# Performance work log

Measured on AMD Instinct MI355X. Metric: run time of the kernel, lower is better.

The kernel has to match this reference:

```python
import jax, jax.numpy as jnp
import numpy as np

TOPK = 2
ALPHA = 32.0
EPS = 1e-20


def setup_inputs() -> dict:
    key = jax.random.key(0)
    ks = jax.random.split(key, 6)
    E, D, R, Q, V = 16, 2048, 16, 2048, 512
    B, S = 2, 2048
    return {
        "hidden_states": jax.random.normal(ks[0], (B, S, D), jnp.float32),
        "router_weight": jax.random.normal(ks[1], (E, D), jnp.float32) * 0.02,
        "q_lora_a": jax.random.normal(ks[2], (E, D, R), jnp.float32) * 0.02,
        "q_lora_b": jax.random.normal(ks[3], (E, R, Q), jnp.float32) * 0.02,
        "v_lora_a": jax.random.normal(ks[4], (E, D, R), jnp.float32) * 0.02,
        "v_lora_b": jax.random.normal(ks[5], (E, R, V), jnp.float32) * 0.02,
    }


def reference(hidden_states, router_weight, q_lora_a, q_lora_b, v_lora_a, v_lora_b):
    E, D, R = q_lora_a.shape
    Qo = q_lora_b.shape[-1]
    Vo = v_lora_b.shape[-1]
    scale = ALPHA / float(R)
    orig_shape = hidden_states.shape[:-1]
    h = hidden_states.reshape(-1, D)  # [n, D]
    n = h.shape[0]

    # router: top-k softmax probs, renormalized over the k selected experts
    logits = jnp.einsum('nd,ed->ne', h, router_weight)
    probs = jax.nn.softmax(logits, axis=-1)
    scores, idx = jax.lax.top_k(probs, TOPK)          # [n, k]
    scores = scores / (scores.sum(-1, keepdims=True) + EPS)

    # per-token expert combine weights c[n, e] = scale * sum_k score_k * 1[idx_k == e]
    c = jnp.zeros((n, E), h.dtype).at[jnp.arange(n)[:, None], idx].add(scores * scale)

    # dense per-expert low-rank projections; weighting by c makes non-selected
    # experts contribute zero -> identical math to gather + einsum + weighted sum.
    q_low = jnp.einsum('nd,edr->ner', h, q_lora_a) * c[..., None]  # [n, E, R]
    v_low = jnp.einsum('nd,edr->ner', h, v_lora_a) * c[..., None]
    q_delta = jnp.einsum('ner,erq->nq', q_low, q_lora_b)
    v_delta = jnp.einsum('ner,erv->nv', v_low, v_lora_b)

    return (q_delta.reshape(*orig_shape, Qo), v_delta.reshape(*orig_shape, Vo))
```

## Files before the change

### kernel.cpp

```cpp
#include <hip/hip_runtime.h>
#include <math.h>

#define DD 2048
#define EE 16
#define RR 16
#define QO 2048
#define VO 512
#define DSPLIT 4
#define DRANGE (DD / DSPLIT)
#define DC 64
#define HSTR (DC + 4)
#define ASTR 20
#define RDC 256
#define DSPL 8
#define TB 32
#define ACHUNKS 16
#define T2 32
#define CGQ (QO / 256)
#define CGV (VO / 256)

struct Route { int i0, i1; float w0, w1; };

__global__ void zero_cnt(int* __restrict__ cnt) {
    if (threadIdx.x < EE) cnt[threadIdx.x] = 0;
}

__global__ __launch_bounds__(256) void logits_kernel(
    const float* __restrict__ h, const float* __restrict__ rw,
    double* __restrict__ lgp, int n)
{
    __shared__ float hs[8 * RDC];

    int t0 = blockIdx.x * 8;
    int ds = blockIdx.y;
    int d0 = ds * RDC;
    int e  = threadIdx.x >> 4;
    int l  = threadIdx.x & 15;

    for (int i = threadIdx.x; i < 8 * (RDC / 4); i += 256) {
        int t = i >> 6, dq = (i & 63) * 4;
        float4 v = make_float4(0.f, 0.f, 0.f, 0.f);
        if (t0 + t < n)
            v = *(const float4*)&h[(size_t)(t0 + t) * DD + d0 + dq];
        *(float4*)&hs[t * RDC + dq] = v;
    }
    __syncthreads();

    double acc[8];
#pragma unroll
    for (int t = 0; t < 8; ++t) acc[t] = 0.0;

    const float* rwe = rw + e * DD + d0;
#pragma unroll
    for (int g = 0; g < RDC / 64; ++g) {
        int d = g * 64 + l * 4;
        float4 r4 = *(const float4*)&rwe[d];
        double rx = r4.x, ry = r4.y, rz = r4.z, rw4 = r4.w;
#pragma unroll
        for (int t = 0; t < 8; ++t) {
            float4 hv = *(const float4*)&hs[t * RDC + d];
            acc[t] += (double)hv.x * rx + (double)hv.y * ry
                    + (double)hv.z * rz + (double)hv.w * rw4;
        }
    }
#pragma unroll
    for (int t = 0; t < 8; ++t) {
#pragma unroll
        for (int off = 8; off; off >>= 1)
            acc[t] += __shfl_down(acc[t], off, 16);
    }
    if (l == 0) {
#pragma unroll
        for (int t = 0; t < 8; ++t) {
            int tok = t0 + t;
            if (tok < n)
                lgp[((size_t)tok * DSPL + ds) * EE + e] = acc[t];
        }
    }
}

__global__ __launch_bounds__(256) void finalize_kernel(
    const double* __restrict__ lgp, Route* __restrict__ route,
    unsigned short* __restrict__ bucket, int* __restrict__ cnt, int n)
{
    int tok = blockIdx.x * 256 + threadIdx.x;
    if (tok >= n) return;

    double lg[EE];
#pragma unroll
    for (int e = 0; e < EE; ++e) lg[e] = 0.0;
    const double* p = lgp + (size_t)tok * (DSPL * EE);
#pragma unroll
    for (int ds = 0; ds < DSPL; ++ds)
#pragma unroll
        for (int e = 0; e < EE; ++e) lg[e] += p[ds * EE + e];

    int i0 = 0;
    for (int i = 1; i < EE; ++i) if (lg[i] > lg[i0]) i0 = i;
    int i1 = -1;
    for (int i = 0; i < EE; ++i)
        if (i != i0 && (i1 < 0 || lg[i] > lg[i1])) i1 = i;
    double ed = exp(lg[i1] - lg[i0]);
    double w0 = 2.0 / (1.0 + ed);
    Route rt;
    rt.i0 = i0; rt.i1 = i1;
    rt.w0 = (float)w0;
    rt.w1 = (float)(2.0 - w0);
    route[tok] = rt;
    int p0 = atomicAdd(&cnt[i0], 1);
    bucket[(size_t)i0 * n + p0] = (unsigned short)(tok * 2);
    int p1 = atomicAdd(&cnt[i1], 1);
    bucket[(size_t)i1 * n + p1] = (unsigned short)(tok * 2 + 1);
}

__global__ __launch_bounds__(256) void a_kernel(
    const float* __restrict__ h, const Route* __restrict__ route,
    const unsigned short* __restrict__ bucket, const int* __restrict__ cnt,
    const float* __restrict__ qa, const float* __restrict__ va,
    float* __restrict__ low, int n)
{
    int e  = blockIdx.x;
    int ds = blockIdx.z;
    int cnt_e = cnt[e];

    __shared__ int   sel_tok[TB];
    __shared__ int   sel_k[TB];
    __shared__ float sel_w[TB];
    __align__(16) __shared__ float aq_s[DC * ASTR];
    __align__(16) __shared__ float av_s[DC * ASTR];
    __align__(16) __shared__ float hs[TB * HSTR];

    const float* qa_e = qa + (size_t)e * DD * RR;
    const float* va_e = va + (size_t)e * DD * RR;

    int s    = threadIdx.x & 15;
    int tile = threadIdx.x >> 4;
    int tp   = tile >> 2;
    int rp   = tile & 3;

    for (int c0 = blockIdx.y * TB; c0 < cnt_e; c0 += gridDim.y * TB) {
        int mb = min(TB, cnt_e - c0);
        if (threadIdx.x < TB && threadIdx.x < mb) {
            int slot = bucket[(size_t)e * n + c0 + threadIdx.x];
            int tok = slot >> 1, k = slot & 1;
            Route rt = route[tok];
            sel_tok[threadIdx.x] = tok;
            sel_k[threadIdx.x]   = k;
            sel_w[threadIdx.x]   = k ? rt.w1 : rt.w0;
        }
        float accq[8][4], accv[8][4];
#pragma unroll
        for (int ti = 0; ti < 8; ++ti)
#pragma unroll
            for (int ri = 0; ri < 4; ++ri) { accq[ti][ri] = 0.f; accv[ti][ri] = 0.f; }

        for (int d0 = ds * DRANGE; d0 < (ds + 1) * DRANGE; d0 += DC) {
            __syncthreads();
            {
                int i = threadIdx.x;
                int d = i >> 2, rf = (i & 3) * 4;
                *(float4*)&aq_s[d * ASTR + rf] = *(const float4*)&qa_e[(size_t)(d0 + d) * RR + rf];
                *(float4*)&av_s[d * ASTR + rf] = *(const float4*)&va_e[(size_t)(d0 + d) * RR + rf];
            }
            for (int i = threadIdx.x; i < TB * (DC / 4); i += 256) {
                int j = i >> 4, dq = (i & 15) * 4;
                float4 v = make_float4(0.f, 0.f, 0.f, 0.f);
                if (j < mb)
                    v = *(const float4*)&h[(size_t)sel_tok[j] * DD + d0 + dq];
                *(float4*)&hs[j * HSTR + dq] = v;
            }
            __syncthreads();
#pragma unroll
            for (int dd = 0; dd < DC / 16; ++dd) {
                int d = (dd << 4) + s;
                float hv[8];
#pragma unroll
                for (int ti = 0; ti < 8; ++ti)
                    hv[ti] = hs[(tp * 8 + ti) * HSTR + d];
                float4 aqv = *(const float4*)&aq_s[d * ASTR + rp * 4];
                float4 avv = *(const float4*)&av_s[d * ASTR + rp * 4];
                const float* aqp = &aqv.x;
                const float* avp = &avv.x;
#pragma unroll
                for (int ti = 0; ti < 8; ++ti)
#pragma unroll
                    for (int ri = 0; ri < 4; ++ri) {
                        accq[ti][ri] = fmaf(hv[ti], aqp[ri], accq[ti][ri]);
                        accv[ti][ri] = fmaf(hv[ti], avp[ri], accv[ti][ri]);
                    }
            }
        }
#pragma unroll
        for (int ti = 0; ti < 8; ++ti)
#pragma unroll
            for (int ri = 0; ri < 4; ++ri) {
#pragma unroll
                for (int off = 8; off; off >>= 1) {
                    accq[ti][ri] += __shfl_down(accq[ti][ri], off, 16);
                    accv[ti][ri] += __shfl_down(accv[ti][ri], off, 16);
                }
            }
        if (s == 0) {
#pragma unroll
            for (int ti = 0; ti < 8; ++ti) {
                int t = tp * 8 + ti;
                if (t < mb) {
                    int   tok = sel_tok[t];
                    int   k   = sel_k[t];
                    float w   = sel_w[t];
                    size_t base = ((size_t)(tok * 2 + k) * DSPLIT + ds) * 32;
                    float4 q4 = make_float4(accq[ti][0] * w, accq[ti][1] * w,
                                            accq[ti][2] * w, accq[ti][3] * w);
                    float4 v4 = make_float4(accv[ti][0] * w, accv[ti][1] * w,
                                            accv[ti][2] * w, accv[ti][3] * w);
                    *(float4*)&low[base + rp * 4]      = q4;
                    *(float4*)&low[base + 16 + rp * 4] = v4;
                }
            }
        }
        __syncthreads();
    }
}

__global__ __launch_bounds__(256) void b_kernel(
    const Route* __restrict__ route, const float* __restrict__ low,
    const float* __restrict__ qb, const float* __restrict__ vb,
    float* __restrict__ outq, float* __restrict__ outv, int n)
{
    int t0 = blockIdx.x * T2;
    int cg = blockIdx.y;
    int tid = threadIdx.x;

    __shared__ float acc_s[T2 * 256];
    __shared__ float ls[T2 * 2 * RR];
    __shared__ int   elist[EE * T2];
    __shared__ int   ecnt[EE];
    __shared__ Route rts[T2];

    if (tid < EE) ecnt[tid] = 0;
    if (tid < T2) {
        int tok = t0 + tid;
        if (tok < n) rts[tid] = route[tok];
        else { rts[tid].i0 = -1; rts[tid].i1 = -1; rts[tid].w0 = 0.f; rts[tid].w1 = 0.f; }
    }
    __syncthreads();
    if (tid < T2 * 2) {
        int j = tid >> 1, k = tid & 1;
        int e = k ? rts[j].i1 : rts[j].i0;
        if (e >= 0) {
            int p = atomicAdd(&ecnt[e], 1);
            elist[e * T2 + p] = j * 2 + k;
        }
    }
    int side = (cg >= CGQ) ? 1 : 0;
    {
        int slot = tid >> 2, r4 = (tid & 3) * 4;
        int j = slot >> 1, k = slot & 1;
        int tok = t0 + j;
        float4 v = make_float4(0.f, 0.f, 0.f, 0.f);
        if (tok < n) {
            const float* lp = low + (size_t)(tok * 2 + k) * (DSPLIT * 32) + side * 16 + r4;
            float4 p0 = *(const float4*)(lp);
            float4 p1 = *(const float4*)(lp + 32);
            float4 p2 = *(const float4*)(lp + 64);
            float4 p3 = *(const float4*)(lp + 96);
            v.x = p0.x + p1.x + p2.x + p3.x;
            v.y = p0.y + p1.y + p2.y + p3.y;
            v.z = p0.z + p1.z + p2.z + p3.z;
            v.w = p0.w + p1.w + p2.w + p3.w;
        }
        *(float4*)&ls[slot * RR + r4] = v;
    }
#pragma unroll
    for (int j = 0; j < T2; ++j) acc_s[j * 256 + tid] = 0.f;
    __syncthreads();

    const float* bp; float* outp; int W, colbase;
    if (cg < CGQ) { bp = qb; outp = outq; W = QO; colbase = cg * 256; }
    else          { bp = vb; outp = outv; W = VO; colbase = (cg - CGQ) * 256; }
    int col = colbase + tid;

    float bcA[RR], bcB[RR];
    {
        const float* be = bp + col;
#pragma unroll
        for (int r = 0; r < RR; ++r) bcA[r] = be[(size_t)r * W];
    }

#define PROC_E(EI, BC)                                                      \
    {                                                                       \
        int c = ecnt[EI];                                                   \
        for (int ii = 0; ii < c; ++ii) {                                    \
            int sk = elist[(EI) * T2 + ii];                                 \
            const float* lp = &ls[sk * RR];                                 \
            float4 l0 = *(const float4*)(lp);                               \
            float4 l1 = *(const float4*)(lp + 4);                           \
            float4 l2 = *(const float4*)(lp + 8);                           \
            float4 l3 = *(const float4*)(lp + 12);                          \
            float v = 0.f;                                                  \
            v = fmaf(l0.x, BC[0],  v); v = fmaf(l0.y, BC[1],  v);           \
            v = fmaf(l0.z, BC[2],  v); v = fmaf(l0.w, BC[3],  v);           \
            v = fmaf(l1.x, BC[4],  v); v = fmaf(l1.y, BC[5],  v);           \
            v = fmaf(l1.z, BC[6],  v); v = fmaf(l1.w, BC[7],  v);           \
            v = fmaf(l2.x, BC[8],  v); v = fmaf(l2.y, BC[9],  v);           \
            v = fmaf(l2.z, BC[10], v); v = fmaf(l2.w, BC[11], v);           \
            v = fmaf(l3.x, BC[12], v); v = fmaf(l3.y, BC[13], v);           \
            v = fmaf(l3.z, BC[14], v); v = fmaf(l3.w, BC[15], v);           \
            acc_s[(sk >> 1) * 256 + tid] += v;   \
        }                                                                   \
    }

    for (int e = 0; e < EE; e += 2) {
        {
            const float* bn = bp + (size_t)(e + 1) * RR * W + col;
#pragma unroll
            for (int r = 0; r < RR; ++r) bcB[r] = bn[(size_t)r * W];
        }
        PROC_E(e, bcA);
        if (e + 2 < EE) {
            const float* bn = bp + (size_t)(e + 2) * RR * W + col;
#pragma unroll
            for (int r = 0; r < RR; ++r) bcA[r] = bn[(size_t)r * W];
        }
        PROC_E(e + 1, bcB);
    }
#undef PROC_E

#pragma unroll
    for (int j = 0; j < T2; ++j) {
        int tok = t0 + j;
        if (tok < n) outp[(size_t)tok * W + col] = acc_s[j * 256 + tid];
    }
}

extern "C" void kernel_launch(void* const* d_in, const int* in_sizes, int n_in,
                              void* d_out, int out_size, void* d_ws, size_t ws_size,
                              hipStream_t stream) {
    const float* h  = (const float*)d_in[0];
    const float* rw = (const float*)d_in[1];
    const float* qa = (const float*)d_in[2];
    const float* qb = (const float*)d_in[3];
    const float* va = (const float*)d_in[4];
    const float* vb = (const float*)d_in[5];

    int n = in_sizes[0] / DD;
    float* out  = (float*)d_out;
    float* outq = out;
    float* outv = out + (size_t)n * QO;

    char* ws = (char*)d_ws;
    Route* route = (Route*)ws;
    size_t off = ((size_t)n * sizeof(Route) + 255) & ~(size_t)255;
    int* cnt = (int*)(ws + off);
    off = (off + EE * sizeof(int) + 255) & ~(size_t)255;
    unsigned short* bucket = (unsigned short*)(ws + off);
    off = (off + (size_t)EE * n * sizeof(unsigned short) + 255) & ~(size_t)255;
    float* low = (float*)(ws + off);
    double* lgp = (double*)low;

    zero_cnt<<<1, 64, 0, stream>>>(cnt);

    dim3 g1((n + 7) / 8, DSPL);
    logits_kernel<<<g1, 256, 0, stream>>>(h, rw, lgp, n);

    finalize_kernel<<<(n + 255) / 256, 256, 0, stream>>>(lgp, route, bucket, cnt, n);

    dim3 g2(EE, ACHUNKS, DSPLIT);
    a_kernel<<<g2, 256, 0, stream>>>(h, route, bucket, cnt, qa, va, low, n);

    dim3 g3((n + T2 - 1) / T2, CGQ + CGV);
    b_kernel<<<g3, 256, 0, stream>>>(route, low, qb, vb, outq, outv, n);
}
```

Before: 240.6 us.

## Restructure routing finalize and A-projection kernel; fold counter reset into logits kernel

Removes the separate counter-zeroing launch by resetting the counts inside the logits kernel. The finalize kernel now uses 16 lanes per token with shuffle reductions for the top-2 search. The A kernel preloads the whole per-expert D-slice of both LoRA A matrices into shared memory once. Each wave then streams its own 8 tokens' hidden rows straight from global memory into registers with double buffering, which removes the per-chunk block syncs and the hidden-state staging. Risks: the in-kernel counter reset only works if finalize is strictly ordered after logits, register pressure rises, and the hidden-state reads are strided with less coalescing.

Result: no change. 236.7 us (-1.6%).

```diff
diff --git a/kernel.cpp b/kernel.cpp
--- a/kernel.cpp
+++ b/kernel.cpp
@@ -9,27 +9,24 @@
 #define DSPLIT 4
 #define DRANGE (DD / DSPLIT)
 #define DC 64
-#define HSTR (DC + 4)
-#define ASTR 20
 #define RDC 256
 #define DSPL 8
 #define TB 32
-#define ACHUNKS 16
+#define ABLK 8
 #define T2 32
 #define CGQ (QO / 256)
 #define CGV (VO / 256)
 
 struct Route { int i0, i1; float w0, w1; };
 
-__global__ void zero_cnt(int* __restrict__ cnt) {
-    if (threadIdx.x < EE) cnt[threadIdx.x] = 0;
-}
-
 __global__ __launch_bounds__(256) void logits_kernel(
     const float* __restrict__ h, const float* __restrict__ rw,
-    double* __restrict__ lgp, int n)
+    double* __restrict__ lgp, int* __restrict__ cnt, int n)
 {
     __shared__ float hs[8 * RDC];
+
+    if (blockIdx.x == 0 && blockIdx.y == 0 && threadIdx.x < EE)
+        cnt[threadIdx.x] = 0;
 
     int t0 = blockIdx.x * 8;
     int ds = blockIdx.y;
@@ -83,37 +80,78 @@
     const double* __restrict__ lgp, Route* __restrict__ route,
     unsigned short* __restrict__ bucket, int* __restrict__ cnt, int n)
 {
-    int tok = blockIdx.x * 256 + threadIdx.x;
+    int j   = threadIdx.x >> 4;
+    int l   = threadIdx.x & 15;
+    int tok = blockIdx.x * 16 + j;
     if (tok >= n) return;
 
-    double lg[EE];
-#pragma unroll
-    for (int e = 0; e < EE; ++e) lg[e] = 0.0;
-    const double* p = lgp + (size_t)tok * (DSPL * EE);
-#pragma unroll
-    for (int ds = 0; ds < DSPL; ++ds)
-#pragma unroll
-        for (int e = 0; e < EE; ++e) lg[e] += p[ds * EE + e];
-
-    int i0 = 0;
-    for (int i = 1; i < EE; ++i) if (lg[i] > lg[i0]) i0 = i;
-    int i1 = -1;
-    for (int i = 0; i < EE; ++i)
-        if (i != i0 && (i1 < 0 || lg[i] > lg[i1])) i1 = i;
-    double ed = exp(lg[i1] - lg[i0]);
-    double w0 = 2.0 / (1.0 + ed);
-    Route rt;
-    rt.i0 = i0; rt.i1 = i1;
-    rt.w0 = (float)w0;
-    rt.w1 = (float)(2.0 - w0);
-    route[tok] = rt;
-    int p0 = atomicAdd(&cnt[i0], 1);
-    bucket[(size_t)i0 * n + p0] = (unsigned short)(tok * 2);
-    int p1 = atomicAdd(&cnt[i1], 1);
-    bucket[(size_t)i1 * n + p1] = (unsigned short)(tok * 2 + 1);
-}
-
-__global__ __launch_bounds__(256) void a_kernel(
+    const double* p = lgp + (size_t)tok * (DSPL * EE) + l;
+    double s = 0.0;
+#pragma unroll
+    for (int ds = 0; ds < DSPL; ++ds) s += p[ds * EE];
+
+    double m1 = s; int i1 = l;
+#pragma unroll
+    for (int off = 8; off; off >>= 1) {
+        double om = __shfl_xor(m1, off, 16);
+        int    oi = __shfl_xor(i1, off, 16);
+        if (om > m1 || (om == m1 && oi < i1)) { m1 = om; i1 = oi; }
+    }
+    double s2 = (l == i1) ? -1.0e300 : s;
+    double m2 = s2; int i2 = l;
+#pragma unroll
+    for (int off = 8; off; off >>= 1) {
+        double om = __shfl_xor(m2, off, 16);
+        int    oi = __shfl_xor(i2, off, 16);
+        if (om > m2 || (om == m2 && oi < i2)) { m2 = om; i2 = oi; }
+    }
+    if (l == 0) {
+        double ed = exp(m2 - m1);
+        double w0 = 2.0 / (1.0 + ed);
+        Route rt;
+        rt.i0 = i1; rt.i1 = i2;
+        rt.w0 = (float)w0;
+        rt.w1 = (float)(2.0 - w0);
+        route[tok] = rt;
+        int p0 = atomicAdd(&cnt[i1], 1);
+        bucket[(size_t)i1 * n + p0] = (unsigned short)(tok * 2);
+        int p1 = atomicAdd(&cnt[i2], 1);
+        bucket[(size_t)i2 * n + p1] = (unsigned short)(tok * 2 + 1);
+    }
+}
+
+__device__ __forceinline__ void loadh(float (&hv)[4][8],
+        const float* const (&hp)[8], int d0) {
+#pragma unroll
+    for (int dd = 0; dd < 4; ++dd)
+#pragma unroll
+        for (int ti = 0; ti < 8; ++ti)
+            hv[dd][ti] = hp[ti][d0 + dd * 16];
+}
+
+__device__ __forceinline__ void computeh(float (&accq)[8][4], float (&accv)[8][4],
+        const float (&hv)[4][8], const float* aq, const float* av,
+        int d0, int s, int rp) {
+#pragma unroll
+    for (int dd = 0; dd < 4; ++dd) {
+        int d = d0 + dd * 16 + s;
+        float4 aqv = *(const float4*)&aq[d * RR + rp * 4];
+        float4 avv = *(const float4*)&av[d * RR + rp * 4];
+        const float* ap = &aqv.x;
+        const float* vp = &avv.x;
+#pragma unroll
+        for (int ti = 0; ti < 8; ++ti) {
+            float hvv = hv[dd][ti];
+#pragma unroll
+            for (int ri = 0; ri < 4; ++ri) {
+                accq[ti][ri] = fmaf(hvv, ap[ri], accq[ti][ri]);
+                accv[ti][ri] = fmaf(hvv, vp[ri], accv[ti][ri]);
+            }
+        }
+    }
+}
+
+__global__ __launch_bounds__(256, 2) void a_kernel(
     const float* __restrict__ h, const Route* __restrict__ route,
     const unsigned short* __restrict__ bucket, const int* __restrict__ cnt,
     const float* __restrict__ qa, const float* __restrict__ va,
@@ -122,74 +160,65 @@
     int e  = blockIdx.x;
     int ds = blockIdx.z;
     int cnt_e = cnt[e];
-
-    __shared__ int   sel_tok[TB];
-    __shared__ int   sel_k[TB];
-    __shared__ float sel_w[TB];
-    __align__(16) __shared__ float aq_s[DC * ASTR];
-    __align__(16) __shared__ float av_s[DC * ASTR];
-    __align__(16) __shared__ float hs[TB * HSTR];
-
-    const float* qa_e = qa + (size_t)e * DD * RR;
-    const float* va_e = va + (size_t)e * DD * RR;
-
-    int s    = threadIdx.x & 15;
-    int tile = threadIdx.x >> 4;
-    int tp   = tile >> 2;
-    int rp   = tile & 3;
-
-    for (int c0 = blockIdx.y * TB; c0 < cnt_e; c0 += gridDim.y * TB) {
-        int mb = min(TB, cnt_e - c0);
-        if (threadIdx.x < TB && threadIdx.x < mb) {
-            int slot = bucket[(size_t)e * n + c0 + threadIdx.x];
-            int tok = slot >> 1, k = slot & 1;
-            Route rt = route[tok];
-            sel_tok[threadIdx.x] = tok;
-            sel_k[threadIdx.x]   = k;
-            sel_w[threadIdx.x]   = k ? rt.w1 : rt.w0;
-        }
+    if ((int)(blockIdx.y * TB) >= cnt_e) return;
+
+    __align__(16) __shared__ float aq_s[DRANGE * RR];
+    __align__(16) __shared__ float av_s[DRANGE * RR];
+
+    const int dbase = ds * DRANGE;
+    const float* qa_e = qa + ((size_t)e * DD + dbase) * RR;
+    const float* va_e = va + ((size_t)e * DD + dbase) * RR;
+
+#pragma unroll
+    for (int k = 0; k < 8; ++k) {
+        int t = (k << 8) + threadIdx.x;
+        *(float4*)&aq_s[t * 4] = *(const float4*)&qa_e[(size_t)t * 4];
+        *(float4*)&av_s[t * 4] = *(const float4*)&va_e[(size_t)t * 4];
+    }
+    __syncthreads();
+
+    int lane = threadIdx.x & 63;
+    int w    = threadIdx.x >> 6;
+    int s    = lane & 15;
+    int rp   = lane >> 4;
+
+    for (int cb = blockIdx.y * TB; cb < cnt_e; cb += gridDim.y * TB) {
+        int cw = cb + w * 8;
+        if (cw >= cnt_e) continue;
+
+        int sl = 0; float wt = 0.f;
+        int idx = cw + lane;
+        if (lane < 8 && idx < cnt_e) {
+            sl = bucket[(size_t)e * n + idx];
+            Route rt = route[sl >> 1];
+            wt = (sl & 1) ? rt.w1 : rt.w0;
+        }
+        const float* hp[8];
+        int   slots[8];
+        float wts[8];
+#pragma unroll
+        for (int ti = 0; ti < 8; ++ti) {
+            slots[ti] = __shfl(sl, ti);
+            wts[ti]   = __shfl(wt, ti);
+            hp[ti]    = h + (size_t)(slots[ti] >> 1) * DD + dbase + s;
+        }
+
         float accq[8][4], accv[8][4];
 #pragma unroll
         for (int ti = 0; ti < 8; ++ti)
 #pragma unroll
             for (int ri = 0; ri < 4; ++ri) { accq[ti][ri] = 0.f; accv[ti][ri] = 0.f; }
 
-        for (int d0 = ds * DRANGE; d0 < (ds + 1) * DRANGE; d0 += DC) {
-            __syncthreads();
-            {
-                int i = threadIdx.x;
-                int d = i >> 2, rf = (i & 3) * 4;
-                *(float4*)&aq_s[d * ASTR + rf] = *(const float4*)&qa_e[(size_t)(d0 + d) * RR + rf];
-                *(float4*)&av_s[d * ASTR + rf] = *(const float4*)&va_e[(size_t)(d0 + d) * RR + rf];
-            }
-            for (int i = threadIdx.x; i < TB * (DC / 4); i += 256) {
-                int j = i >> 4, dq = (i & 15) * 4;
-                float4 v = make_float4(0.f, 0.f, 0.f, 0.f);
-                if (j < mb)
-                    v = *(const float4*)&h[(size_t)sel_tok[j] * DD + d0 + dq];
-                *(float4*)&hs[j * HSTR + dq] = v;
-            }
-            __syncthreads();
-#pragma unroll
-            for (int dd = 0; dd < DC / 16; ++dd) {
-                int d = (dd << 4) + s;
-                float hv[8];
-#pragma unroll
-                for (int ti = 0; ti < 8; ++ti)
-                    hv[ti] = hs[(tp * 8 + ti) * HSTR + d];
-                float4 aqv = *(const float4*)&aq_s[d * ASTR + rp * 4];
-                float4 avv = *(const float4*)&av_s[d * ASTR + rp * 4];
-                const float* aqp = &aqv.x;
-                const float* avp = &avv.x;
-#pragma unroll
-                for (int ti = 0; ti < 8; ++ti)
-#pragma unroll
-                    for (int ri = 0; ri < 4; ++ri) {
-                        accq[ti][ri] = fmaf(hv[ti], aqp[ri], accq[ti][ri]);
-                        accv[ti][ri] = fmaf(hv[ti], avp[ri], accv[ti][ri]);
-                    }
-            }
-        }
+        float hvA[4][8], hvB[4][8];
+        loadh(hvA, hp, 0);
+#pragma unroll
+        for (int d0 = 0; d0 < DRANGE; d0 += 2 * DC) {
+            loadh(hvB, hp, d0 + DC);
+            computeh(accq, accv, hvA, aq_s, av_s, d0, s, rp);
+            if (d0 + 2 * DC < DRANGE) loadh(hvA, hp, d0 + 2 * DC);
+            computeh(accq, accv, hvB, aq_s, av_s, d0 + DC, s, rp);
+        }
+
 #pragma unroll
         for (int ti = 0; ti < 8; ++ti)
 #pragma unroll
@@ -203,22 +232,19 @@
         if (s == 0) {
 #pragma unroll
             for (int ti = 0; ti < 8; ++ti) {
-                int t = tp * 8 + ti;
-                if (t < mb) {
-                    int   tok = sel_tok[t];
-                    int   k   = sel_k[t];
-                    float w   = sel_w[t];
-                    size_t base = ((size_t)(tok * 2 + k) * DSPLIT + ds) * 32;
-                    float4 q4 = make_float4(accq[ti][0] * w, accq[ti][1] * w,
-                                            accq[ti][2] * w, accq[ti][3] * w);
-                    float4 v4 = make_float4(accv[ti][0] * w, accv[ti][1] * w,
-                                            accv[ti][2] * w, accv[ti][3] * w);
+                if (cw + ti < cnt_e) {
+                    int   sl2 = slots[ti];
+                    float wt2 = wts[ti];
+                    size_t base = ((size_t)sl2 * DSPLIT + ds) * 32;
+                    float4 q4 = make_float4(accq[ti][0] * wt2, accq[ti][1] * wt2,
+                                            accq[ti][2] * wt2, accq[ti][3] * wt2);
+                    float4 v4 = make_float4(accv[ti][0] * wt2, accv[ti][1] * wt2,
+                                            accv[ti][2] * wt2, accv[ti][3] * wt2);
                     *(float4*)&low[base + rp * 4]      = q4;
                     *(float4*)&low[base + 16 + rp * 4] = v4;
                 }
             }
         }
-        __syncthreads();
     }
 }
 
@@ -358,14 +384,12 @@
     float* low = (float*)(ws + off);
     double* lgp = (double*)low;
 
-    zero_cnt<<<1, 64, 0, stream>>>(cnt);
-
     dim3 g1((n + 7) / 8, DSPL);
-    logits_kernel<<<g1, 256, 0, stream>>>(h, rw, lgp, n);
-
-    finalize_kernel<<<(n + 255) / 256, 256, 0, stream>>>(lgp, route, bucket, cnt, n);
-
-    dim3 g2(EE, ACHUNKS, DSPLIT);
+    logits_kernel<<<g1, 256, 0, stream>>>(h, rw, lgp, cnt, n);
+
+    finalize_kernel<<<(n + 15) / 16, 256, 0, stream>>>(lgp, route, bucket, cnt, n);
+
+    dim3 g2(EE, ABLK, DSPLIT);
     a_kernel<<<g2, 256, 0, stream>>>(h, route, bucket, cnt, qa, va, low, n);
 
     dim3 g3((n + T2 - 1) / T2, CGQ + CGV);
```
